# Optimization experiments

Measured on AMD Instinct MI355X. Metric: run time of the kernel, lower is better.

## Reference

```python
import jax, jax.numpy as jnp
import numpy as np

B, S, D, H, E = 2, 2048, 1024, 4096, 8


def setup_inputs() -> dict:
    key = jax.random.key(0)
    k0, k1, k2, k3 = jax.random.split(key, 4)
    x = jax.random.normal(k0, (B, S, D), dtype=jnp.float32)
    router_w = jax.random.normal(k1, (E, D), dtype=jnp.float32) * 0.02   # Top2Router Linear weight [E, D]
    w1 = jax.random.normal(k2, (E, D, H), dtype=jnp.float32) * 0.02      # stacked fc1 weights (transposed: x @ w1[e])
    w2 = jax.random.normal(k3, (E, H, D), dtype=jnp.float32) * 0.02      # stacked fc2 weights
    return {"x": x, "router_w": router_w, "w1": w1, "w2": w2}


def reference(x, router_w, w1, w2):
    # x: [B, S, D] -> flatten tokens. Single-rank EP: all-to-all is identity,
    # microbatch split is a pure overlap trick, per-token math unchanged.
    b, s, d = x.shape
    e = router_w.shape[0]
    xf = x.reshape(-1, d)                                     # [T, D]
    # Top-2 router with renormalized gate weights
    probs = jax.nn.softmax(xf @ router_w.T, axis=-1)          # [T, E]
    topv, topi = jax.lax.top_k(probs, 2)                      # [T, 2]
    topv = topv / (topv.sum(axis=-1, keepdims=True) + 1e-9)
    # Combine weights per expert: cw[t,e] = sum_k topv[t,k] * [topi[t,k]==e]
    cw = (jax.nn.one_hot(topi, e, dtype=xf.dtype) * topv[..., None]).sum(axis=1)  # [T, E]
    # Expert MLPs (dense-over-experts reference for the grouped GEMM)
    h = jax.nn.gelu(jnp.einsum('td,edh->teh', xf, w1), approximate=False)  # [T, E, H]
    y = jnp.einsum('teh,ehd->ted', h, w2)                                   # [T, E, D]
    out = jnp.einsum('te,ted->td', cw, y)                                   # weighted combine (scatter-add equiv.)
    return out.reshape(b, s, d)
```

## Files before the change

### kernel.cpp

```cpp
#include <hip/hip_runtime.h>

#define T_TOK 4096
#define DIM   1024
#define HID   4096
#define NEXP  8
#define MAXROWS 9216

typedef unsigned short u16;
typedef __attribute__((ext_vector_type(8))) short short8;
typedef __attribute__((ext_vector_type(4))) float f32x4;
typedef __attribute__((ext_vector_type(4))) unsigned short u16x4;
typedef __attribute__((ext_vector_type(8))) unsigned short u16x8;

typedef __attribute__((address_space(3))) unsigned int lds_uint;
typedef const __attribute__((address_space(1))) unsigned int gbl_uint;

__device__ __forceinline__ u16 f2bf(float f) {
    union { float f; unsigned int u; } v; v.f = f;
    unsigned int r = v.u + 0x7fffu + ((v.u >> 16) & 1u);
    return (u16)(r >> 16);
}

__device__ __forceinline__ float gelu_f(float v) {
    float u = 1.5957691216f * (v + 0.044715f * v * v * v);
    float s = 1.0f / (1.0f + __expf(-u));
    return v * s;
}

__global__ __launch_bounds__(256)
void transpose_cast2(const float* __restrict__ w1, u16* __restrict__ w1t,
                     const float* __restrict__ w2, u16* __restrict__ w2t,
                     int* __restrict__ counts) {
    int b = blockIdx.x;
    if (b == 0 && threadIdx.x < NEXP) counts[threadIdx.x] = 0;
    const float* in; u16* out; int R, C, bx, by, e;
    if (b < 8192) {
        e = b >> 10; int t = b & 1023; bx = t & 63; by = t >> 6;
        in = w1; out = w1t; R = DIM; C = HID;
    } else {
        b -= 8192;
        e = b >> 10; int t = b & 1023; bx = t & 15; by = t >> 4;
        in = w2; out = w2t; R = HID; C = DIM;
    }
    __shared__ u16 t[64 * 68];
    size_t mo = (size_t)e * DIM * HID;
    const float* ip = in + mo;
    u16* op = out + mo;
    int c0 = bx * 64, r0 = by * 64;
    int tid = threadIdx.x;
#pragma unroll
    for (int j = 0; j < 4; ++j) {
        int id = tid + 256 * j;
        int r = id >> 4, cc = id & 15;
        f32x4 v = *(const f32x4*)(ip + (size_t)(r0 + r) * C + c0 + 4 * cc);
        u16x4 w; w.x = f2bf(v.x); w.y = f2bf(v.y); w.z = f2bf(v.z); w.w = f2bf(v.w);
        *(u16x4*)(t + r * 68 + 4 * cc) = w;
    }
    __syncthreads();
#pragma unroll
    for (int j = 0; j < 4; ++j) {
        int id = tid + 256 * j;
        int c = id >> 4, rj = id & 15;
        u16x4 o;
        o.x = t[(4 * rj + 0) * 68 + c];
        o.y = t[(4 * rj + 1) * 68 + c];
        o.z = t[(4 * rj + 2) * 68 + c];
        o.w = t[(4 * rj + 3) * 68 + c];
        *(u16x4*)(op + (size_t)(c0 + c) * R + r0 + 4 * rj) = o;
    }
}

__global__ __launch_bounds__(256)
void router_k(const float* __restrict__ x, const float* __restrict__ rw,
              int* __restrict__ counts, int* __restrict__ tE,
              int* __restrict__ tS, float* __restrict__ tG) {
    int wave = threadIdx.x >> 6, lane = threadIdx.x & 63;
    int t = blockIdx.x * 4 + wave;
    const float* xr = x + (size_t)t * DIM;
    float xv[16];
#pragma unroll
    for (int i = 0; i < 16; ++i) xv[i] = xr[lane + 64*i];
    float lg[NEXP];
#pragma unroll
    for (int e = 0; e < NEXP; ++e) {
        const float* wr_ = rw + e * DIM;
        float a = 0.f;
#pragma unroll
        for (int i = 0; i < 16; ++i) a += xv[i] * wr_[lane + 64*i];
        lg[e] = a;
    }
#pragma unroll
    for (int off = 32; off > 0; off >>= 1)
#pragma unroll
        for (int e = 0; e < NEXP; ++e) lg[e] += __shfl_xor(lg[e], off, 64);
    if (lane == 0) {
        float mx = lg[0];
        for (int e = 1; e < NEXP; ++e) mx = fmaxf(mx, lg[e]);
        float p[NEXP], s = 0.f;
        for (int e = 0; e < NEXP; ++e) { p[e] = expf(lg[e] - mx); s += p[e]; }
        float inv_s = 1.f / s;
        for (int e = 0; e < NEXP; ++e) p[e] *= inv_s;
        int i0 = 0;
        for (int e = 1; e < NEXP; ++e) if (p[e] > p[i0]) i0 = e;
        int i1 = (i0 == 0) ? 1 : 0;
        for (int e = 0; e < NEXP; ++e) if (e != i0 && p[e] > p[i1]) i1 = e;
        float v0 = p[i0], v1 = p[i1];
        float inv = 1.f / (v0 + v1 + 1e-9f);
        int s0 = atomicAdd(&counts[i0], 1);
        int s1 = atomicAdd(&counts[i1], 1);
        tE[2*t] = i0;  tE[2*t+1] = i1;
        tS[2*t] = s0;  tS[2*t+1] = s1;
        tG[2*t] = v0 * inv;  tG[2*t+1] = v1 * inv;
    }
}

__device__ __forceinline__ int pbase_of(const int* __restrict__ counts, int e) {
    int pb = 0;
#pragma unroll
    for (int i = 0; i < NEXP; ++i) {
        int pad = ((counts[i] + 127) >> 7) << 7;
        pb += (i < e) ? pad : 0;
    }
    return pb;
}

__global__ __launch_bounds__(256)
void gather_k(const float* __restrict__ x, const int* __restrict__ tE,
              const int* __restrict__ tS, const int* __restrict__ counts,
              u16* __restrict__ xg) {
    int a = blockIdx.x;
    int t = a >> 1, k = a & 1;
    int e = tE[2*t + k];
    int row = pbase_of(counts, e) + tS[2*t + k];
    const f32x4* xr = (const f32x4*)(x + (size_t)t * DIM);
    u16x4* o = (u16x4*)(xg + (size_t)row * DIM);
    int i = threadIdx.x;
    f32x4 v = xr[i];
    u16x4 r; r.x = f2bf(v.x); r.y = f2bf(v.y); r.z = f2bf(v.z); r.w = f2bf(v.w);
    o[i] = r;
}

template<int K, int KSPLIT, bool GELU, typename OutT>
__global__ __launch_bounds__(256)
void gemm_bt(const u16* __restrict__ A, const u16* __restrict__ BtAll,
             OutT* __restrict__ C, const int* __restrict__ counts,
             int N, size_t cstride) {
    int e  = blockIdx.z / KSPLIT;
    int ks = blockIdx.z % KSPLIT;
    int cnt = counts[e];
    int mt = blockIdx.y;
    if (mt * 128 >= cnt) return;
    int row0 = pbase_of(counts, e) + mt * 128;
    const u16* Bt = BtAll + (size_t)e * N * K;
    OutT* Cp = C + (size_t)ks * cstride;
    int col0 = blockIdx.x * 128;
    const int kb0 = ks * (K / KSPLIT);
    constexpr int KITER = K / KSPLIT / 64;

    __shared__ __align__(16) u16 smem[128 * 128];
    u16* As = smem;
    u16* Bs = smem + 128 * 64;

    int tid = threadIdx.x;
    int lane = tid & 63;
    int w = tid >> 6;
    int quad = lane >> 4, m16 = lane & 15;
    int wr = (w >> 1) * 64, wc = (w & 1) * 64;
    int rsub = lane >> 3;
    int kch  = lane & 7;
    int kchs = kch ^ rsub;

    const u16* ga[4];
    const u16* gb[4];
#pragma unroll
    for (int i = 0; i < 4; ++i) {
        int r = (w * 4 + i) * 8 + rsub;
        ga[i] = A  + (size_t)(row0 + r) * K + kb0 + kchs * 8;
        gb[i] = Bt + (size_t)(col0 + r) * K + kb0 + kchs * 8;
    }
    int sw = m16 & 7;
    const u16* aP0 = As + (wr + m16) * 64 + ((quad       ^ sw) << 3);
    const u16* aP1 = As + (wr + m16) * 64 + (((4 + quad) ^ sw) << 3);
    const u16* bP0 = Bs + (wc + m16) * 64 + ((quad       ^ sw) << 3);
    const u16* bP1 = Bs + (wc + m16) * 64 + (((4 + quad) ^ sw) << 3);

    f32x4 acc[4][4] = {};

    for (int kit = 0; kit < KITER; ++kit) {
#pragma unroll
        for (int i = 0; i < 4; ++i) {
            int grp = w * 4 + i;
            __builtin_amdgcn_global_load_lds((gbl_uint*)ga[i], (lds_uint*)(As + grp * 512), 16, 0, 0);
            __builtin_amdgcn_global_load_lds((gbl_uint*)gb[i], (lds_uint*)(Bs + grp * 512), 16, 0, 0);
            ga[i] += 64; gb[i] += 64;
        }
        __syncthreads();
        {
            short8 af[4], bfr[4];
#pragma unroll
            for (int mi = 0; mi < 4; ++mi) af[mi]  = *(const short8*)(aP0 + mi * 1024);
#pragma unroll
            for (int ni = 0; ni < 4; ++ni) bfr[ni] = *(const short8*)(bP0 + ni * 1024);
#pragma unroll
            for (int mi = 0; mi < 4; ++mi)
#pragma unroll
                for (int ni = 0; ni < 4; ++ni)
                    acc[mi][ni] = __builtin_amdgcn_mfma_f32_16x16x32_bf16(af[mi], bfr[ni], acc[mi][ni], 0, 0, 0);
#pragma unroll
            for (int mi = 0; mi < 4; ++mi) af[mi]  = *(const short8*)(aP1 + mi * 1024);
#pragma unroll
            for (int ni = 0; ni < 4; ++ni) bfr[ni] = *(const short8*)(bP1 + ni * 1024);
#pragma unroll
            for (int mi = 0; mi < 4; ++mi)
#pragma unroll
                for (int ni = 0; ni < 4; ++ni)
                    acc[mi][ni] = __builtin_amdgcn_mfma_f32_16x16x32_bf16(af[mi], bfr[ni], acc[mi][ni], 0, 0, 0);
        }
        __syncthreads();
    }

    if (GELU) {
#pragma unroll
        for (int mi = 0; mi < 4; ++mi) {
#pragma unroll
            for (int r = 0; r < 4; ++r) {
                int row = wr + mi * 16 + quad * 4 + r;
#pragma unroll
                for (int ni = 0; ni < 4; ++ni) {
                    int col = wc + ni * 16 + m16;
                    int c16 = col >> 3, w8 = col & 7;
                    smem[row * 128 + (((c16 ^ (row & 15)) << 3) | w8)] = f2bf(gelu_f(acc[mi][ni][r]));
                }
            }
        }
        __syncthreads();
        int row_b = tid >> 4, c16_b = tid & 15;
        const u16* ls = smem + row_b * 128 + (((c16_b ^ (row_b & 15)) << 3));
        u16* gp = (u16*)Cp + (size_t)(row0 + row_b) * N + col0 + c16_b * 8;
#pragma unroll
        for (int j = 0; j < 8; ++j) {
            *(u16x8*)gp = *(const u16x8*)ls;
            ls += 16 * 128;
            gp += (size_t)16 * N;
        }
    } else {
        float* gp = (float*)Cp + (size_t)(row0 + wr + quad * 4) * N + col0 + wc + m16;
#pragma unroll
        for (int mi = 0; mi < 4; ++mi)
#pragma unroll
            for (int r = 0; r < 4; ++r) {
                float* rp = gp + (size_t)(mi * 16 + r) * N;
#pragma unroll
                for (int ni = 0; ni < 4; ++ni)
                    rp[ni * 16] = acc[mi][ni][r];
            }
    }
}

__global__ __launch_bounds__(256)
void combine_k(const float* __restrict__ p0, const float* __restrict__ p1,
               const int* __restrict__ tE, const int* __restrict__ tS,
               const float* __restrict__ tG, const int* __restrict__ counts,
               float* __restrict__ out) {
    int t = blockIdx.x;
    int e0 = tE[2*t], e1 = tE[2*t+1];
    int r0 = pbase_of(counts, e0) + tS[2*t];
    int r1 = pbase_of(counts, e1) + tS[2*t+1];
    float g0 = tG[2*t], g1 = tG[2*t+1];
    int i = threadIdx.x;
    f32x4 a0 = ((const f32x4*)(p0 + (size_t)r0 * DIM))[i];
    f32x4 b0 = ((const f32x4*)(p1 + (size_t)r0 * DIM))[i];
    f32x4 a1 = ((const f32x4*)(p0 + (size_t)r1 * DIM))[i];
    f32x4 b1 = ((const f32x4*)(p1 + (size_t)r1 * DIM))[i];
    f32x4* o = (f32x4*)(out + (size_t)t * DIM);
    o[i] = g0 * (a0 + b0) + g1 * (a1 + b1);
}

extern "C" void kernel_launch(void* const* d_in, const int* in_sizes, int n_in,
                              void* d_out, int out_size, void* d_ws, size_t ws_size,
                              hipStream_t stream) {
    const float* x  = (const float*)d_in[0];
    const float* rw = (const float*)d_in[1];
    const float* w1 = (const float*)d_in[2];
    const float* w2 = (const float*)d_in[3];
    float* out = (float*)d_out;

    char* ws = (char*)d_ws;
    u16* w1t = (u16*)(ws + 0);
    u16* xg  = (u16*)(ws + 67108864ull);
    u16* w2t = (u16*)(ws + 85983232ull);
    u16* hb  = (u16*)(ws + 153092096ull);
    float* p0 = (float*)(ws + 0);
    float* p1 = (float*)(ws + 37748736ull);
    int* ctrl   = (int*)(ws + 228589568ull);
    int* counts = ctrl;
    int* tE     = ctrl + 32;
    int* tS     = ctrl + 32 + 8192;
    float* tG   = (float*)(ctrl + 32 + 16384);

    transpose_cast2<<<16384, 256, 0, stream>>>(w1, w1t, w2, w2t, counts);
    router_k<<<T_TOK / 4, 256, 0, stream>>>(x, rw, counts, tE, tS, tG);
    gather_k<<<T_TOK * 2, 256, 0, stream>>>(x, tE, tS, counts, xg);
    gemm_bt<DIM, 1, true, u16><<<dim3(HID / 128, 10, NEXP), 256, 0, stream>>>(
        xg, w1t, hb, counts, HID, 0);
    gemm_bt<HID, 2, false, float><<<dim3(DIM / 128, 10, NEXP * 2), 256, 0, stream>>>(
        hb, w2t, p0, counts, DIM, (size_t)MAXROWS * DIM);
    combine_k<<<T_TOK, 256, 0, stream>>>(p0, p1, tE, tS, tG, counts, out);
}
```

Before: 670.7 us.

## Pre-tile expert weights into contiguous 128x64 blocks and interleave experts in grid

The weight transpose/cast kernel now writes each expert weight as contiguous 128-column by 64-k tiles of 8192 elements, so each GEMM k-step reads one contiguous 16KB block instead of 128 strided rows. The GEMM grid is flattened to 1D with the expert index in the low bits, which spreads the experts' tiles across CUs and balances work when expert token counts differ. The cost is a more complex index computation and a different write pattern in the transpose kernel, which now stores 16-byte vectors contiguously.

```diff
diff --git a/kernel.cpp b/kernel.cpp
--- a/kernel.cpp
+++ b/kernel.cpp
@@ -28,45 +28,42 @@
 }
 
 __global__ __launch_bounds__(256)
-void transpose_cast2(const float* __restrict__ w1, u16* __restrict__ w1t,
-                     const float* __restrict__ w2, u16* __restrict__ w2t,
-                     int* __restrict__ counts) {
+void transpose_blocked(const float* __restrict__ w1, u16* __restrict__ w1t,
+                       const float* __restrict__ w2, u16* __restrict__ w2t,
+                       int* __restrict__ counts) {
     int b = blockIdx.x;
     if (b == 0 && threadIdx.x < NEXP) counts[threadIdx.x] = 0;
-    const float* in; u16* out; int R, C, bx, by, e;
-    if (b < 8192) {
-        e = b >> 10; int t = b & 1023; bx = t & 63; by = t >> 6;
-        in = w1; out = w1t; R = DIM; C = HID;
+    const float* in; u16* out; int C, KT, ct, kt, e;
+    if (b < 4096) {
+        e = b >> 9; int t = b & 511; ct = t & 31; kt = t >> 5;
+        in = w1; out = w1t; C = HID; KT = 16;
     } else {
-        b -= 8192;
-        e = b >> 10; int t = b & 1023; bx = t & 15; by = t >> 4;
-        in = w2; out = w2t; R = HID; C = DIM;
-    }
-    __shared__ u16 t[64 * 68];
+        b -= 4096;
+        e = b >> 9; int t = b & 511; ct = t & 7; kt = t >> 3;
+        in = w2; out = w2t; C = DIM; KT = 64;
+    }
+    __shared__ u16 tl[64 * 130];
     size_t mo = (size_t)e * DIM * HID;
-    const float* ip = in + mo;
-    u16* op = out + mo;
-    int c0 = bx * 64, r0 = by * 64;
+    const float* ip = in + mo + (size_t)(kt * 64) * C + ct * 128;
+    u16* op = out + mo + (size_t)(ct * KT + kt) * 8192;
     int tid = threadIdx.x;
+#pragma unroll
+    for (int j = 0; j < 8; ++j) {
+        int id = tid + 256 * j;
+        int kr = id >> 5, cg = id & 31;
+        f32x4 v = *(const f32x4*)(ip + (size_t)kr * C + 4 * cg);
+        u16x4 w; w.x = f2bf(v.x); w.y = f2bf(v.y); w.z = f2bf(v.z); w.w = f2bf(v.w);
+        *(u16x4*)(tl + kr * 130 + 4 * cg) = w;
+    }
+    __syncthreads();
 #pragma unroll
     for (int j = 0; j < 4; ++j) {
         int id = tid + 256 * j;
-        int r = id >> 4, cc = id & 15;
-        f32x4 v = *(const f32x4*)(ip + (size_t)(r0 + r) * C + c0 + 4 * cc);
-        u16x4 w; w.x = f2bf(v.x); w.y = f2bf(v.y); w.z = f2bf(v.z); w.w = f2bf(v.w);
-        *(u16x4*)(t + r * 68 + 4 * cc) = w;
-    }
-    __syncthreads();
-#pragma unroll
-    for (int j = 0; j < 4; ++j) {
-        int id = tid + 256 * j;
-        int c = id >> 4, rj = id & 15;
-        u16x4 o;
-        o.x = t[(4 * rj + 0) * 68 + c];
-        o.y = t[(4 * rj + 1) * 68 + c];
-        o.z = t[(4 * rj + 2) * 68 + c];
-        o.w = t[(4 * rj + 3) * 68 + c];
-        *(u16x4*)(op + (size_t)(c0 + c) * R + r0 + 4 * rj) = o;
+        int n = id >> 3, c = id & 7;
+        u16x8 o;
+#pragma unroll
+        for (int m = 0; m < 8; ++m) o[m] = tl[(c * 8 + m) * 130 + n];
+        *(u16x8*)(op + id * 8) = o;
     }
 }
 
@@ -140,21 +137,26 @@
     o[i] = r;
 }
 
-template<int K, int KSPLIT, bool GELU, typename OutT>
+template<int K, int KSPLIT, int NX, bool GELU, typename OutT>
 __global__ __launch_bounds__(256)
 void gemm_bt(const u16* __restrict__ A, const u16* __restrict__ BtAll,
              OutT* __restrict__ C, const int* __restrict__ counts,
              int N, size_t cstride) {
-    int e  = blockIdx.z / KSPLIT;
-    int ks = blockIdx.z % KSPLIT;
+    int lin = blockIdx.x;
+    int e = lin & 7;
+    int kk = lin >> 3;
+    int ct = kk % NX;
+    int rest = kk / NX;
+    int ks = rest % KSPLIT;
+    int mt = rest / KSPLIT;
     int cnt = counts[e];
-    int mt = blockIdx.y;
     if (mt * 128 >= cnt) return;
     int row0 = pbase_of(counts, e) + mt * 128;
     const u16* Bt = BtAll + (size_t)e * N * K;
     OutT* Cp = C + (size_t)ks * cstride;
-    int col0 = blockIdx.x * 128;
+    int col0 = ct * 128;
     const int kb0 = ks * (K / KSPLIT);
+    constexpr int KT = K / 64;
     constexpr int KITER = K / KSPLIT / 64;
 
     __shared__ __align__(16) u16 smem[128 * 128];
@@ -176,7 +178,7 @@
     for (int i = 0; i < 4; ++i) {
         int r = (w * 4 + i) * 8 + rsub;
         ga[i] = A  + (size_t)(row0 + r) * K + kb0 + kchs * 8;
-        gb[i] = Bt + (size_t)(col0 + r) * K + kb0 + kchs * 8;
+        gb[i] = Bt + ((size_t)ct * KT + kb0 / 64) * 8192 + r * 64 + kchs * 8;
     }
     int sw = m16 & 7;
     const u16* aP0 = As + (wr + m16) * 64 + ((quad       ^ sw) << 3);
@@ -192,7 +194,7 @@
             int grp = w * 4 + i;
             __builtin_amdgcn_global_load_lds((gbl_uint*)ga[i], (lds_uint*)(As + grp * 512), 16, 0, 0);
             __builtin_amdgcn_global_load_lds((gbl_uint*)gb[i], (lds_uint*)(Bs + grp * 512), 16, 0, 0);
-            ga[i] += 64; gb[i] += 64;
+            ga[i] += 64; gb[i] += 8192;
         }
         __syncthreads();
         {
@@ -298,12 +300,12 @@
     int* tS     = ctrl + 32 + 8192;
     float* tG   = (float*)(ctrl + 32 + 16384);
 
-    transpose_cast2<<<16384, 256, 0, stream>>>(w1, w1t, w2, w2t, counts);
+    transpose_blocked<<<8192, 256, 0, stream>>>(w1, w1t, w2, w2t, counts);
     router_k<<<T_TOK / 4, 256, 0, stream>>>(x, rw, counts, tE, tS, tG);
     gather_k<<<T_TOK * 2, 256, 0, stream>>>(x, tE, tS, counts, xg);
-    gemm_bt<DIM, 1, true, u16><<<dim3(HID / 128, 10, NEXP), 256, 0, stream>>>(
+    gemm_bt<DIM, 1, 32, true, u16><<<2560, 256, 0, stream>>>(
         xg, w1t, hb, counts, HID, 0);
-    gemm_bt<HID, 2, false, float><<<dim3(DIM / 128, 10, NEXP * 2), 256, 0, stream>>>(
+    gemm_bt<HID, 2, 8, false, float><<<1280, 256, 0, stream>>>(
         hb, w2t, p0, counts, DIM, (size_t)MAXROWS * DIM);
     combine_k<<<T_TOK, 256, 0, stream>>>(p0, p1, tE, tS, tG, counts, out);
 }
```

New measurement: 645.4 us. -3.8%, faster.
